# Optimization experiments

Hardware: AMD Instinct MI355X
Metric: run time of the kernel (lower is better)

The kernel has to match this reference:

```python
import jax, jax.numpy as jnp
import numpy as np

S, B, D, H = 1024, 8, 768, 12
PROMPT_NUM = 8
DH = D // H


def setup_inputs() -> dict:
    key = jax.random.key(0)
    ks = jax.random.split(key, 5)
    scale = 1.0 / np.sqrt(D)
    return {
        "x": jax.random.normal(ks[0], (S, B, D), dtype=jnp.float32),
        "in_proj_weight": jax.random.normal(ks[1], (3 * D, D), dtype=jnp.float32) * scale,
        "in_proj_bias": jax.random.normal(ks[2], (3 * D,), dtype=jnp.float32) * 0.02,
        "out_w": jax.random.normal(ks[3], (D, D), dtype=jnp.float32) * scale,
        "out_b": jax.random.normal(ks[4], (D,), dtype=jnp.float32) * 0.02,
    }


def reference(x, in_proj_weight, in_proj_bias, out_w, out_b):
    # x: (S, B, D) -> (B, S, D)
    xt = jnp.transpose(x, (1, 0, 2))
    qkv = xt @ in_proj_weight.T + in_proj_bias  # (B, S, 3D)
    q, k, v = jnp.split(qkv, 3, axis=-1)
    q = q.reshape(B, S, H, DH)
    k = k.reshape(B, S, H, DH)
    v = v.reshape(B, S, H, DH)
    # affinity (n, q, k, h); scale by sqrt(head_dim)
    aff = jnp.einsum("nqhc,nkhc->nqkh", q / np.sqrt(DH), k)
    # prompt masking: CLS_MASK | PROMPT_MASK
    tokens = S - PROMPT_NUM
    m = np.zeros((S, S), dtype=bool)
    m[0, tokens:] = True          # CLS_MASK: CLS query can't attend to prompts
    m[tokens:, tokens:] = True    # PROMPT_MASK: prompts can't attend to prompts
    m = jnp.asarray(m)
    aff = jnp.where(m[None, :, :, None], jnp.float32(-10000.0), aff)
    # softmax over key axis (dim=-2 of nqkh)
    aff = jax.nn.softmax(aff, axis=2)
    mix = jnp.einsum("nqlh,nlhc->nqhc", aff, v)  # (B, S, H, DH)
    out = mix.reshape(B, S, D) @ out_w.T + out_b
    # transpose back to (S, B, ...)
    return (
        jnp.transpose(q, (1, 0, 2, 3)),
        jnp.transpose(k, (1, 0, 2, 3)),
        jnp.transpose(v, (1, 0, 2, 3)),
        jnp.transpose(out, (1, 0, 2)),
    )
```

## Files before the change

kernel.cpp:

```cpp
#include <hip/hip_runtime.h>
#include <hip/hip_bf16.h>


typedef unsigned short u16;
typedef __attribute__((ext_vector_type(8))) short short8;
typedef __attribute__((ext_vector_type(4))) short short4v;
typedef __attribute__((ext_vector_type(4))) float floatx4;
typedef __attribute__((ext_vector_type(4))) unsigned short ushort4v;
typedef __attribute__((ext_vector_type(2))) unsigned int uint2v;

#define NB 8
#define NS 1024
#define NH 12
#define ND 768
#define DHD 64
#define TOKENS 1016
#define QKV_OUT_STRIDE 6291456

#if __has_builtin(__builtin_amdgcn_exp2f)
#define EXP2(x) __builtin_amdgcn_exp2f(x)
#else
#define EXP2(x) exp2f(x)
#endif

#if defined(__HIP_DEVICE_COMPILE__)
  #if __has_builtin(__builtin_amdgcn_mfma_f32_16x16x16bf16_1k)
    #define MFMA16(a, b, c) __builtin_amdgcn_mfma_f32_16x16x16bf16_1k(a, b, c, 0, 0, 0)
  #else
    #define MFMA16(a, b, c) __builtin_amdgcn_mfma_f32_16x16x16_bf16(a, b, c, 0, 0, 0)
  #endif
  #define GLD16(g, l)                                                        \
    __builtin_amdgcn_global_load_lds(                                        \
        (const __attribute__((address_space(1))) void*)(g),                  \
        (__attribute__((address_space(3))) void*)(l), 16, 0, 0)
#else
  #define MFMA16(a, b, c) (c)
  #define GLD16(g, l) ((void)0)
#endif

__device__ __forceinline__ u16 f2bf(float f) {
  union { float f; unsigned u; } c; c.f = f;
  return (u16)((c.u + 0x7fffu + ((c.u >> 16) & 1u)) >> 16);
}

#define CVT_B0 6144
#define CVT_B1 1728
#define CVT_B2 576
__global__ __launch_bounds__(256) void cvt3(
    const float* __restrict__ s0, u16* __restrict__ d0,
    const float* __restrict__ s1, u16* __restrict__ d1,
    const float* __restrict__ s2, u16* __restrict__ d2) {
  int blk = blockIdx.x;
  const float* s; u16* d;
  if (blk < CVT_B0) { s = s0; d = d0; }
  else if (blk < CVT_B0 + CVT_B1) { s = s1; d = d1; blk -= CVT_B0; }
  else { s = s2; d = d2; blk -= CVT_B0 + CVT_B1; }
  const int i = (blk * 256 + (int)threadIdx.x) * 4;
  const float4 v = *(const float4*)(s + i);
  ushort4v o;
  o.x = f2bf(v.x); o.y = f2bf(v.y); o.z = f2bf(v.z); o.w = f2bf(v.w);
  *(ushort4v*)(d + i) = o;
}

#define GEMM_STAGE(buf, k0)                                                  \
  do {                                                                       \
    GLD16(ga0 + (k0), &buf##A[c0 * 16][0]);                                  \
    GLD16(ga1 + (k0), &buf##A[c0 * 16 + 16][0]);                             \
    GLD16(gb0 + (k0), &buf##B[c0 * 16][0]);                                  \
    GLD16(gb1 + (k0), &buf##B[c0 * 16 + 16][0]);                             \
  } while (0)

#define GEMM_COMPUTE(buf)                                                    \
  do {                                                                       \
    short8 af[4], bfr[4];                                                    \
    _Pragma("unroll")                                                        \
    for (int mt = 0; mt < 4; ++mt)                                           \
      af[mt] = *(const short8*)&buf##A[wm * 64 + mt * 16 + l15][quad * 8];   \
    _Pragma("unroll")                                                        \
    for (int nt = 0; nt < 4; ++nt)                                           \
      bfr[nt] = *(const short8*)&buf##B[wn * 64 + nt * 16 + l15][quad * 8];  \
    _Pragma("unroll")                                                        \
    for (int mt = 0; mt < 4; ++mt)                                           \
      _Pragma("unroll")                                                      \
      for (int nt = 0; nt < 4; ++nt)                                         \
        acc[mt][nt] = __builtin_amdgcn_mfma_f32_16x16x32_bf16(               \
            af[mt], bfr[nt], acc[mt][nt], 0, 0, 0);                          \
  } while (0)

__global__ __launch_bounds__(256) void qkv_gemm(
    const u16* __restrict__ Xb, const u16* __restrict__ Wb,
    const float* __restrict__ bias, float* __restrict__ out) {
  __shared__ __align__(16) u16 p0A[128][32];
  __shared__ __align__(16) u16 p0B[128][32];
  __shared__ __align__(16) u16 p1A[128][32];
  __shared__ __align__(16) u16 p1B[128][32];
  const int tid = threadIdx.x;
  const int lane = tid & 63, wave = tid >> 6;
  const int l15 = lane & 15, quad = lane >> 4;
  const int wm = wave & 1, wn = wave >> 1;
  const int L = (int)blockIdx.x + 64 * (int)blockIdx.y;
  const int xcd = L & 7, i = L >> 3;
  const int mblk = (xcd + 8 * (i & 7)) * 128;
  const int nblk = (i >> 3) * 128;

  floatx4 acc[4][4];
#pragma unroll
  for (int i2 = 0; i2 < 4; ++i2)
#pragma unroll
    for (int j = 0; j < 4; ++j) acc[i2][j] = (floatx4)0.f;

  const int lr = lane >> 2;
  const int lc = (lane & 3) * 8;
  const int c0 = wave * 2;
  const int r0 = c0 * 16 + lr, r1 = r0 + 16;
  const int gm0 = mblk + r0, gm1 = mblk + r1;
  const u16* ga0 = Xb + ((gm0 & 1023) * NB + (gm0 >> 10)) * ND + lc;
  const u16* ga1 = Xb + ((gm1 & 1023) * NB + (gm1 >> 10)) * ND + lc;
  const u16* gb0 = Wb + (nblk + r0) * ND + lc;
  const u16* gb1 = Wb + (nblk + r1) * ND + lc;

  GEMM_STAGE(p0, 0);
  __syncthreads();
  for (int kt = 0; kt < 24; kt += 2) {
    GEMM_STAGE(p1, (kt + 1) * 32);
    GEMM_COMPUTE(p0);
    __syncthreads();
    if (kt + 2 < 24) GEMM_STAGE(p0, (kt + 2) * 32);
    GEMM_COMPUTE(p1);
    __syncthreads();
  }

#pragma unroll
  for (int mt = 0; mt < 4; ++mt) {
#pragma unroll
    for (int r = 0; r < 4; ++r) {
      const int gm = mblk + wm * 64 + mt * 16 + quad * 4 + r;
      const int b = gm >> 10, s = gm & 1023;
#pragma unroll
      for (int nt = 0; nt < 4; ++nt) {
        const int gn = nblk + wn * 64 + nt * 16 + l15;
        const int seg = gn / ND;
        const int nn = gn - seg * ND;
        out[seg * QKV_OUT_STRIDE + (s * NB + b) * ND + nn] = acc[mt][nt][r] + bias[gn];
      }
    }
  }
}

__global__ __launch_bounds__(256) void prep(
    const float* __restrict__ K, const float* __restrict__ V,
    u16* __restrict__ Kb, u16* __restrict__ Vt) {
  __shared__ u16 tile[DHD][40];
  const int t = threadIdx.x;
  const int bh = blockIdx.y;
  const int b = bh / NH, h = bh % NH;
  const int s0 = blockIdx.x * 32;
  const int sl = t >> 3;
  const int c0 = (t & 7) * 8;
  const int s = s0 + sl;
  if (blockIdx.z == 0) {
    const float* src = K + ((s * NB + b) * NH + h) * DHD + c0;
    const float4 v0 = *(const float4*)src;
    const float4 v1 = *(const float4*)(src + 4);
    short8 o;
    o[0] = f2bf(v0.x); o[1] = f2bf(v0.y); o[2] = f2bf(v0.z); o[3] = f2bf(v0.w);
    o[4] = f2bf(v1.x); o[5] = f2bf(v1.y); o[6] = f2bf(v1.z); o[7] = f2bf(v1.w);
    *(short8*)(Kb + ((size_t)bh * NS + s) * DHD + c0) = o;
  } else {
    const float* src = V + ((s * NB + b) * NH + h) * DHD + c0;
    const float4 v0 = *(const float4*)src;
    const float4 v1 = *(const float4*)(src + 4);
    tile[c0 + 0][sl] = f2bf(v0.x); tile[c0 + 1][sl] = f2bf(v0.y);
    tile[c0 + 2][sl] = f2bf(v0.z); tile[c0 + 3][sl] = f2bf(v0.w);
    tile[c0 + 4][sl] = f2bf(v1.x); tile[c0 + 5][sl] = f2bf(v1.y);
    tile[c0 + 6][sl] = f2bf(v1.z); tile[c0 + 7][sl] = f2bf(v1.w);
    __syncthreads();
    const int c = t >> 2;
    const int so = (t & 3) * 8;
    *(short8*)(Vt + ((size_t)bh * DHD + c) * NS + s0 + so) =
        *(const short8*)&tile[c][so];
  }
}

__global__ __launch_bounds__(256) void attn(
    const float* __restrict__ Q, const u16* __restrict__ Kb,
    const u16* __restrict__ Vt, u16* __restrict__ mix) {
  __shared__ __align__(16) u16 Kt[64][72];
  __shared__ __align__(16) u16 Vs[64][72];
  const int tid = threadIdx.x;
  const int lane = tid & 63, wave = tid >> 6;
  const int l15 = lane & 15, quad = lane >> 4;
  const int L = (int)blockIdx.x + 8 * (int)blockIdx.y;
  const int xcd = L & 7, tt = L >> 3;
  const int bh = xcd + 8 * (tt >> 3);
  const int qx = tt & 7;
  const int b = bh / NH, h = bh % NH;
  const int qb = qx * 128 + wave * 32;

  short8 qf[2][2];
  bool qmask[2];
#pragma unroll
  for (int j = 0; j < 2; ++j) {
    const int qj = qb + j * 16 + l15;
    qmask[j] = (qj == 0 || qj >= TOKENS);
    const float* qp = Q + ((qj * NB + b) * NH + h) * DHD + quad * 8;
#pragma unroll
    for (int e = 0; e < 8; ++e) {
      qf[j][0][e] = (short)f2bf(qp[e]);
      qf[j][1][e] = (short)f2bf(qp[32 + e]);
    }
  }

  floatx4 O[2][4];
#pragma unroll
  for (int j = 0; j < 2; ++j)
#pragma unroll
    for (int g = 0; g < 4; ++g) O[j][g] = (floatx4)0.f;
  float li[2] = {0.f, 0.f};

  const u16* kg = Kb + (size_t)bh * NS * DHD;
  const u16* vg = Vt + (size_t)bh * DHD * NS;

  const float C1 = 0.125f * 1.44269504089f;
  const float C0 = -10.0f * 1.44269504089f;

  const int srow = tid >> 2;
  const int scol = (tid & 3) * 16;

  short8 pk0, pk1, pv0, pv1;
  {
    pk0 = *(const short8*)(kg + srow * DHD + scol);
    pk1 = *(const short8*)(kg + srow * DHD + scol + 8);
    pv0 = *(const short8*)(vg + srow * NS + scol);
    pv1 = *(const short8*)(vg + srow * NS + scol + 8);
  }

  for (int it = 0; it < 16; ++it) {
    *(short8*)&Kt[srow][scol] = pk0;
    *(short8*)&Kt[srow][scol + 8] = pk1;
    *(short8*)&Vs[srow][scol] = pv0;
    *(short8*)&Vs[srow][scol + 8] = pv1;
    __syncthreads();
    if (it < 15) {
      const int k0 = (it + 1) * 64;
      pk0 = *(const short8*)(kg + (k0 + srow) * DHD + scol);
      pk1 = *(const short8*)(kg + (k0 + srow) * DHD + scol + 8);
      pv0 = *(const short8*)(vg + srow * NS + k0 + scol);
      pv1 = *(const short8*)(vg + srow * NS + k0 + scol + 8);
    }
    const bool mrow = (it == 15) && (quad >= 2);
#pragma unroll
    for (int sub = 0; sub < 4; ++sub) {
      const short8 kf0 = *(const short8*)&Kt[sub * 16 + l15][quad * 8];
      const short8 kf1 = *(const short8*)&Kt[sub * 16 + l15][32 + quad * 8];
      short4v pb[2];
#pragma unroll
      for (int j = 0; j < 2; ++j) {
        floatx4 a = (floatx4)0.f;
        a = __builtin_amdgcn_mfma_f32_16x16x32_bf16(kf0, qf[j][0], a, 0, 0, 0);
        a = __builtin_amdgcn_mfma_f32_16x16x32_bf16(kf1, qf[j][1], a, 0, 0, 0);
        float p[4];
#pragma unroll
        for (int r = 0; r < 4; ++r) p[r] = EXP2(fmaf(a[r], C1, C0));
        if (sub == 3 && mrow && qmask[j]) {
#pragma unroll
          for (int r = 0; r < 4; ++r) p[r] = 0.f;
        }
        li[j] += (p[0] + p[1]) + (p[2] + p[3]);
        __hip_bfloat162 w0 = __float22bfloat162_rn(make_float2(p[0], p[1]));
        __hip_bfloat162 w1 = __float22bfloat162_rn(make_float2(p[2], p[3]));
        uint2v pw;
        pw.x = *(const unsigned*)&w0;
        pw.y = *(const unsigned*)&w1;
        pb[j] = __builtin_bit_cast(short4v, pw);
      }
#pragma unroll
      for (int g = 0; g < 4; ++g) {
        const short4v vf = *(const short4v*)&Vs[g * 16 + l15][sub * 16 + quad * 4];
        O[0][g] = MFMA16(vf, pb[0], O[0][g]);
        O[1][g] = MFMA16(vf, pb[1], O[1][g]);
      }
    }
    __syncthreads();
  }

#pragma unroll
  for (int j = 0; j < 2; ++j) {
    float l = li[j];
    l += __shfl_xor(l, 16);
    l += __shfl_xor(l, 32);
    const float rl = 1.0f / l;
    const int qj = qb + j * 16 + l15;
    u16* mp = mix + ((size_t)b * NS + qj) * ND + h * DHD + quad * 4;
#pragma unroll
    for (int g = 0; g < 4; ++g) {
      ushort4v o;
#pragma unroll
      for (int r = 0; r < 4; ++r) o[r] = f2bf(O[j][g][r] * rl);
      *(ushort4v*)(mp + g * 16) = o;
    }
  }
}

__global__ __launch_bounds__(256) void out_gemm(
    const u16* __restrict__ A, const u16* __restrict__ Wb,
    const float* __restrict__ bias, float* __restrict__ out) {
  __shared__ __align__(16) u16 p0A[128][32];
  __shared__ __align__(16) u16 p0B[128][32];
  __shared__ __align__(16) u16 p1A[128][32];
  __shared__ __align__(16) u16 p1B[128][32];
  const int tid = threadIdx.x;
  const int lane = tid & 63, wave = tid >> 6;
  const int l15 = lane & 15, quad = lane >> 4;
  const int wm = wave & 1, wn = wave >> 1;
  const int L = (int)blockIdx.x + 64 * (int)blockIdx.y;
  const int xcd = L & 7, i = L >> 3;
  const int mblk = (xcd + 8 * (i & 7)) * 128;
  const int nblk = (i >> 3) * 128;

  floatx4 acc[4][4];
#pragma unroll
  for (int i2 = 0; i2 < 4; ++i2)
#pragma unroll
    for (int j = 0; j < 4; ++j) acc[i2][j] = (floatx4)0.f;

  const int lr = lane >> 2;
  const int lc = (lane & 3) * 8;
  const int c0 = wave * 2;
  const int r0 = c0 * 16 + lr, r1 = r0 + 16;
  const u16* ga0 = A + (mblk + r0) * ND + lc;
  const u16* ga1 = A + (mblk + r1) * ND + lc;
  const u16* gb0 = Wb + (nblk + r0) * ND + lc;
  const u16* gb1 = Wb + (nblk + r1) * ND + lc;

  GEMM_STAGE(p0, 0);
  __syncthreads();
  for (int kt = 0; kt < 24; kt += 2) {
    GEMM_STAGE(p1, (kt + 1) * 32);
    GEMM_COMPUTE(p0);
    __syncthreads();
    if (kt + 2 < 24) GEMM_STAGE(p0, (kt + 2) * 32);
    GEMM_COMPUTE(p1);
    __syncthreads();
  }

#pragma unroll
  for (int mt = 0; mt < 4; ++mt) {
#pragma unroll
    for (int r = 0; r < 4; ++r) {
      const int gm = mblk + wm * 64 + mt * 16 + quad * 4 + r;
      const int b = gm >> 10, s = gm & 1023;
#pragma unroll
      for (int nt = 0; nt < 4; ++nt) {
        const int gn = nblk + wn * 64 + nt * 16 + l15;
        out[(s * NB + b) * ND + gn] = acc[mt][nt][r] + bias[gn];
      }
    }
  }
}

extern "C" void kernel_launch(void* const* d_in, const int* in_sizes, int n_in,
                              void* d_out, int out_size, void* d_ws, size_t ws_size,
                              hipStream_t stream) {
  const float* X  = (const float*)d_in[0];
  const float* W  = (const float*)d_in[1];
  const float* Bi = (const float*)d_in[2];
  const float* Ow = (const float*)d_in[3];
  const float* Ob = (const float*)d_in[4];
  float* out = (float*)d_out;

  u16* Xb  = (u16*)d_ws;
  u16* Wb  = Xb  + 6291456;
  u16* Owb = Wb  + 1769472;
  u16* Vt  = Owb + 589824;
  u16* Kb  = Vt  + 6291456;
  u16* mix = Kb  + 6291456;

  cvt3<<<CVT_B0 + CVT_B1 + CVT_B2, 256, 0, stream>>>(X, Xb, W, Wb, Ow, Owb);
  qkv_gemm<<<dim3(64, 18), 256, 0, stream>>>(Xb, Wb, Bi, out);
  prep<<<dim3(32, 96, 2), 256, 0, stream>>>(out + QKV_OUT_STRIDE,
                                            out + 2 * QKV_OUT_STRIDE, Kb, Vt);
  attn<<<dim3(8, 96), 256, 0, stream>>>(out, Kb, Vt, mix);
  out_gemm<<<dim3(64, 6), 256, 0, stream>>>(mix, Owb, Ob, out + 3 * QKV_OUT_STRIDE);
}
```

Baseline: 246.3 us.

## Enlarge QKV GEMM tile to 256x128 with 512-thread blocks

```diff
diff --git a/kernel.cpp b/kernel.cpp
--- a/kernel.cpp
+++ b/kernel.cpp
@@ -62,23 +62,22 @@
   *(ushort4v*)(d + i) = o;
 }
 
-#define GEMM_STAGE(buf, k0)                                                  \
+#define QKV_STAGE(bufA, bufB, k0)                                            \
   do {                                                                       \
-    GLD16(ga0 + (k0), &buf##A[c0 * 16][0]);                                  \
-    GLD16(ga1 + (k0), &buf##A[c0 * 16 + 16][0]);                             \
-    GLD16(gb0 + (k0), &buf##B[c0 * 16][0]);                                  \
-    GLD16(gb1 + (k0), &buf##B[c0 * 16 + 16][0]);                             \
+    GLD16(ga0 + (k0), &bufA[cA0 * 16][0]);                                   \
+    GLD16(ga1 + (k0), &bufA[cA0 * 16 + 16][0]);                              \
+    GLD16(gb0 + (k0), &bufB[cB * 16][0]);                                    \
   } while (0)
 
-#define GEMM_COMPUTE(buf)                                                    \
+#define QKV_COMPUTE(bufA, bufB)                                              \
   do {                                                                       \
     short8 af[4], bfr[4];                                                    \
     _Pragma("unroll")                                                        \
     for (int mt = 0; mt < 4; ++mt)                                           \
-      af[mt] = *(const short8*)&buf##A[wm * 64 + mt * 16 + l15][quad * 8];   \
+      af[mt] = *(const short8*)&bufA[wm * 64 + mt * 16 + l15][quad * 8];     \
     _Pragma("unroll")                                                        \
     for (int nt = 0; nt < 4; ++nt)                                           \
-      bfr[nt] = *(const short8*)&buf##B[wn * 64 + nt * 16 + l15][quad * 8];  \
+      bfr[nt] = *(const short8*)&bufB[wn * 64 + nt * 16 + l15][quad * 8];    \
     _Pragma("unroll")                                                        \
     for (int mt = 0; mt < 4; ++mt)                                           \
       _Pragma("unroll")                                                      \
@@ -87,21 +86,20 @@
             af[mt], bfr[nt], acc[mt][nt], 0, 0, 0);                          \
   } while (0)
 
-__global__ __launch_bounds__(256) void qkv_gemm(
+__global__ __launch_bounds__(512) void qkv_gemm(
     const u16* __restrict__ Xb, const u16* __restrict__ Wb,
     const float* __restrict__ bias, float* __restrict__ out) {
-  __shared__ __align__(16) u16 p0A[128][32];
+  __shared__ __align__(16) u16 p0A[256][32];
   __shared__ __align__(16) u16 p0B[128][32];
-  __shared__ __align__(16) u16 p1A[128][32];
+  __shared__ __align__(16) u16 p1A[256][32];
   __shared__ __align__(16) u16 p1B[128][32];
   const int tid = threadIdx.x;
   const int lane = tid & 63, wave = tid >> 6;
   const int l15 = lane & 15, quad = lane >> 4;
-  const int wm = wave & 1, wn = wave >> 1;
-  const int L = (int)blockIdx.x + 64 * (int)blockIdx.y;
-  const int xcd = L & 7, i = L >> 3;
-  const int mblk = (xcd + 8 * (i & 7)) * 128;
-  const int nblk = (i >> 3) * 128;
+  const int wm = wave & 3;
+  const int wn = wave >> 2;
+  const int mblk = blockIdx.y * 256;
+  const int nblk = blockIdx.x * 128;
 
   floatx4 acc[4][4];
 #pragma unroll
@@ -111,22 +109,22 @@
 
   const int lr = lane >> 2;
   const int lc = (lane & 3) * 8;
-  const int c0 = wave * 2;
-  const int r0 = c0 * 16 + lr, r1 = r0 + 16;
-  const int gm0 = mblk + r0, gm1 = mblk + r1;
+  const int cA0 = wave * 2;
+  const int cB = wave;
+  const int rA0 = cA0 * 16 + lr, rA1 = rA0 + 16;
+  const int gm0 = mblk + rA0, gm1 = mblk + rA1;
   const u16* ga0 = Xb + ((gm0 & 1023) * NB + (gm0 >> 10)) * ND + lc;
   const u16* ga1 = Xb + ((gm1 & 1023) * NB + (gm1 >> 10)) * ND + lc;
-  const u16* gb0 = Wb + (nblk + r0) * ND + lc;
-  const u16* gb1 = Wb + (nblk + r1) * ND + lc;
-
-  GEMM_STAGE(p0, 0);
+  const u16* gb0 = Wb + (nblk + cB * 16 + lr) * ND + lc;
+
+  QKV_STAGE(p0A, p0B, 0);
   __syncthreads();
   for (int kt = 0; kt < 24; kt += 2) {
-    GEMM_STAGE(p1, (kt + 1) * 32);
-    GEMM_COMPUTE(p0);
-    __syncthreads();
-    if (kt + 2 < 24) GEMM_STAGE(p0, (kt + 2) * 32);
-    GEMM_COMPUTE(p1);
+    QKV_STAGE(p1A, p1B, (kt + 1) * 32);
+    QKV_COMPUTE(p0A, p0B);
+    __syncthreads();
+    if (kt + 2 < 24) QKV_STAGE(p0A, p0B, (kt + 2) * 32);
+    QKV_COMPUTE(p1A, p1B);
     __syncthreads();
   }
 
@@ -302,6 +300,31 @@
   }
 }
 
+#define GEMM_STAGE(buf, k0)                                                  \
+  do {                                                                       \
+    GLD16(ga0 + (k0), &buf##A[c0 * 16][0]);                                  \
+    GLD16(ga1 + (k0), &buf##A[c0 * 16 + 16][0]);                             \
+    GLD16(gb0 + (k0), &buf##B[c0 * 16][0]);                                  \
+    GLD16(gb1 + (k0), &buf##B[c0 * 16 + 16][0]);                             \
+  } while (0)
+
+#define GEMM_COMPUTE(buf)                                                    \
+  do {                                                                       \
+    short8 af[4], bfr[4];                                                    \
+    _Pragma("unroll")                                                        \
+    for (int mt = 0; mt < 4; ++mt)                                           \
+      af[mt] = *(const short8*)&buf##A[wm * 64 + mt * 16 + l15][quad * 8];   \
+    _Pragma("unroll")                                                        \
+    for (int nt = 0; nt < 4; ++nt)                                           \
+      bfr[nt] = *(const short8*)&buf##B[wn * 64 + nt * 16 + l15][quad * 8];  \
+    _Pragma("unroll")                                                        \
+    for (int mt = 0; mt < 4; ++mt)                                           \
+      _Pragma("unroll")                                                      \
+      for (int nt = 0; nt < 4; ++nt)                                         \
+        acc[mt][nt] = __builtin_amdgcn_mfma_f32_16x16x32_bf16(               \
+            af[mt], bfr[nt], acc[mt][nt], 0, 0, 0);                          \
+  } while (0)
+
 __global__ __launch_bounds__(256) void out_gemm(
     const u16* __restrict__ A, const u16* __restrict__ Wb,
     const float* __restrict__ bias, float* __restrict__ out) {
@@ -377,7 +400,7 @@
   u16* mix = Kb  + 6291456;
 
   cvt3<<<CVT_B0 + CVT_B1 + CVT_B2, 256, 0, stream>>>(X, Xb, W, Wb, Ow, Owb);
-  qkv_gemm<<<dim3(64, 18), 256, 0, stream>>>(Xb, Wb, Bi, out);
+  qkv_gemm<<<dim3(18, 32), 512, 0, stream>>>(Xb, Wb, Bi, out);
   prep<<<dim3(32, 96, 2), 256, 0, stream>>>(out + QKV_OUT_STRIDE,
                                             out + 2 * QKV_OUT_STRIDE, Kb, Vt);
   attn<<<dim3(8, 96), 256, 0, stream>>>(out, Kb, Vt, mix);
```

Result: no change. 247.3 us (+0.4%).
